# Kernel optimization log

Hardware: AMD Instinct MI355X
Metric: run time of the kernel (lower is better)

Reference implementation:

```python
import jax, jax.numpy as jnp
import numpy as np

D_MODEL = 128
EXPAND = 8
D_INNER = EXPAND * D_MODEL            # 1024
HEADDIM = D_MODEL                     # headdim = int(in_channels*8/8)
NHEADS = D_INNER // HEADDIM           # 8
D_STATE = 128
D_CONV = 4
CONV_DIM = D_INNER + 2 * D_STATE      # 1280
D_IN_PROJ = 2 * D_INNER + 2 * D_STATE + NHEADS  # 2312
EPS = 1e-5
B_SZ, SEQ = 2, 2048


def setup_inputs() -> dict:
    key = jax.random.key(0)
    ks = jax.random.split(key, 16)
    n = jax.random.normal
    dt_init = jax.random.uniform(ks[4], (NHEADS,), minval=0.001, maxval=0.1)
    return dict(
        hidden_states=n(ks[0], (B_SZ, SEQ, D_MODEL), jnp.float32),
        w_in=n(ks[1], (D_IN_PROJ, D_MODEL), jnp.float32) / np.float32(np.sqrt(D_MODEL)),
        conv_w=n(ks[2], (CONV_DIM, D_CONV), jnp.float32) / np.float32(np.sqrt(D_CONV)),
        conv_b=n(ks[3], (CONV_DIM,), jnp.float32) * 0.01,
        dt_bias=jnp.log(jnp.expm1(dt_init)),  # inverse-softplus init (official)
        A_log=jnp.log(jax.random.uniform(ks[5], (NHEADS,), minval=1.0, maxval=16.0)),
        D_skip=jnp.ones((NHEADS,), jnp.float32),
        gnorm_w=jnp.ones((D_INNER,), jnp.float32),
        w_out=n(ks[6], (D_MODEL, D_INNER), jnp.float32) / np.float32(np.sqrt(D_INNER)),
        ln1_w=jnp.ones((D_MODEL,), jnp.float32),
        ln1_b=jnp.zeros((D_MODEL,), jnp.float32),
        ln2_w=jnp.ones((D_MODEL,), jnp.float32),
        ln2_b=jnp.zeros((D_MODEL,), jnp.float32),
        mlp_w=n(ks[7], (D_MODEL, D_MODEL), jnp.float32) / np.float32(np.sqrt(D_MODEL)),
        mlp_b=jnp.zeros((D_MODEL,), jnp.float32),
    )


def _layer_norm(x, w, b):
    m = x.mean(-1, keepdims=True)
    xc = x - m
    v = (xc * xc).mean(-1, keepdims=True)
    return xc * jax.lax.rsqrt(v + EPS) * w + b


def _mixer(u, w_in, conv_w, conv_b, dt_bias, A_log, D_skip, gnorm_w, w_out):
    b, l, _ = u.shape
    zxbcdt = u @ w_in.T                                    # (b,l,2312)
    z = zxbcdt[..., :D_INNER]                              # gate
    xBC = zxbcdt[..., D_INNER:D_INNER + CONV_DIM]
    dt = jax.nn.softplus(zxbcdt[..., -NHEADS:] + dt_bias)  # (b,l,h)
    # depthwise causal conv1d + SiLU
    xc = jnp.pad(xBC.swapaxes(1, 2), ((0, 0), (0, 0), (D_CONV - 1, 0)))
    xc = jax.lax.conv_general_dilated(xc, conv_w[:, None, :], (1,), 'VALID',
                                      feature_group_count=CONV_DIM)
    xBC = jax.nn.silu((xc + conv_b[None, :, None]).swapaxes(1, 2))
    x = xBC[..., :D_INNER].reshape(b, l, NHEADS, HEADDIM)  # (b,l,h,p)
    Bm = xBC[..., D_INNER:D_INNER + D_STATE]               # (b,l,n), ngroups=1
    Cm = xBC[..., D_INNER + D_STATE:]                      # (b,l,n)
    A = -jnp.exp(A_log)                                    # (h,)
    dA = jnp.exp(dt * A)                                   # (b,l,h)

    def step(S, inp):
        dA_t, dt_t, B_t, C_t, x_t = inp
        S = S * dA_t[:, :, None, None] + jnp.einsum('bh,bhp,bn->bhpn', dt_t, x_t, B_t)
        return S, jnp.einsum('bhpn,bn->bhp', S, C_t)

    S0 = jnp.zeros((b, NHEADS, HEADDIM, D_STATE), u.dtype)
    _, ys = jax.lax.scan(step, S0, (dA.swapaxes(0, 1), dt.swapaxes(0, 1),
                                    Bm.swapaxes(0, 1), Cm.swapaxes(0, 1),
                                    x.swapaxes(0, 1)))
    y = ys.swapaxes(0, 1) + D_skip[None, None, :, None] * x  # skip connection
    y = y.reshape(b, l, D_INNER) * jax.nn.silu(z)            # gated RMSNorm
    y = y * jax.lax.rsqrt((y * y).mean(-1, keepdims=True) + EPS) * gnorm_w
    return y @ w_out.T


def reference(hidden_states, w_in, conv_w, conv_b, dt_bias, A_log, D_skip,
              gnorm_w, w_out, ln1_w, ln1_b, ln2_w, ln2_b, mlp_w, mlp_b):
    residual = hidden_states
    h = _layer_norm(residual, ln1_w, ln1_b)
    h = _mixer(h, w_in, conv_w, conv_b, dt_bias, A_log, D_skip, gnorm_w, w_out)
    residual = h + residual
    h = _layer_norm(residual, ln2_w, ln2_b)
    return h @ mlp_w.T + mlp_b
```

## Files before the change

kernel.cpp:

```cpp
#include <hip/hip_runtime.h>
#include <hip/hip_bf16.h>

#define B_SZ 2
#define SEQ 2048
#define DMODEL 128
#define DINNER 1024
#define NHEADS 8
#define HEADDIM 128
#define DSTATE 128
#define CONVDIM 1280
#define NPROJ 2304
#define NTOK (B_SZ*SEQ)
#define CHUNK 64
#define NCHUNK (SEQ/CHUNK)
#define LDT 72

using bf16_t = __hip_bfloat16;
using short8 = __attribute__((ext_vector_type(8))) short;
using short4v= __attribute__((ext_vector_type(4))) short;
using f32x4  = __attribute__((ext_vector_type(4))) float;

__device__ __forceinline__ float silu_f(float x) { return x / (1.f + expf(-x)); }
__device__ __forceinline__ float bf2f(short s) {
    unsigned u = ((unsigned)(unsigned short)s) << 16;
    return __uint_as_float(u);
}
__device__ __forceinline__ short f2bf_s(float f) {
    bf16_t h = __float2bfloat16(f);
    return *(short*)&h;
}

__global__ __launch_bounds__(256) void cast3(const float* __restrict__ a, int na,
                                             const float* __restrict__ b, int nb,
                                             const float* __restrict__ c, int nc,
                                             bf16_t* __restrict__ oa,
                                             bf16_t* __restrict__ ob,
                                             bf16_t* __restrict__ oc) {
    int i = blockIdx.x * 256 + threadIdx.x;
    if (i < na) oa[i] = __float2bfloat16(a[i]);
    else if (i < na + nb) ob[i - na] = __float2bfloat16(b[i - na]);
    else if (i < na + nb + nc) oc[i - na - nb] = __float2bfloat16(c[i - na - nb]);
}

__global__ __launch_bounds__(128) void ln_ker(const float* __restrict__ x,
                                              const float* __restrict__ w,
                                              const float* __restrict__ b,
                                              float* __restrict__ out_f,
                                              bf16_t* __restrict__ out_b) {
    int m = blockIdx.x, t = threadIdx.x;
    __shared__ float red[128];
    float v = x[(size_t)m*DMODEL + t];
    red[t] = v; __syncthreads();
    for (int s = 64; s > 0; s >>= 1) { if (t < s) red[t] += red[t+s]; __syncthreads(); }
    float mean = red[0] * (1.f/128.f);
    __syncthreads();
    float xc = v - mean;
    red[t] = xc * xc; __syncthreads();
    for (int s = 64; s > 0; s >>= 1) { if (t < s) red[t] += red[t+s]; __syncthreads(); }
    float var = red[0] * (1.f/128.f);
    float o = xc * rsqrtf(var + 1e-5f) * w[t] + b[t];
    out_f[(size_t)m*DMODEL + t] = o;
    out_b[(size_t)m*DMODEL + t] = __float2bfloat16(o);
}

__global__ __launch_bounds__(256) void gemm_bf(const bf16_t* __restrict__ A,
                                               const bf16_t* __restrict__ W,
                                               bf16_t* __restrict__ C,
                                               int M, int N, int K) {
    int tid = threadIdx.x;
    int wave = tid >> 6, lane = tid & 63;
    int m0 = blockIdx.x * 64 + wave * 16;
    int n0 = blockIdx.y * 64;
    int lr = lane & 15, quad = lane >> 4;
    f32x4 acc[4];
#pragma unroll
    for (int j = 0; j < 4; j++) acc[j] = (f32x4){0.f, 0.f, 0.f, 0.f};
    for (int k0 = 0; k0 < K; k0 += 32) {
        short8 a = *(const short8*)(A + (size_t)(m0 + lr)*K + k0 + quad*8);
#pragma unroll
        for (int j = 0; j < 4; j++) {
            short8 b = *(const short8*)(W + (size_t)(n0 + j*16 + lr)*K + k0 + quad*8);
            acc[j] = __builtin_amdgcn_mfma_f32_16x16x32_bf16(a, b, acc[j], 0, 0, 0);
        }
    }
#pragma unroll
    for (int j = 0; j < 4; j++)
#pragma unroll
        for (int r = 0; r < 4; r++) {
            int row = m0 + quad*4 + r;
            int col = n0 + j*16 + lr;
            C[(size_t)row*N + col] = __float2bfloat16(acc[j][r]);
        }
}

__global__ __launch_bounds__(256) void dt_ker(const float* __restrict__ h,
                                              const float* __restrict__ w_in,
                                              const float* __restrict__ dt_bias,
                                              const float* __restrict__ A_log,
                                              float* __restrict__ dt,
                                              float* __restrict__ ldA) {
    int idx = blockIdx.x * 256 + threadIdx.x;
    if (idx >= NTOK * NHEADS) return;
    int m = idx >> 3, hd = idx & 7;
    const float* hr = h + (size_t)m * DMODEL;
    const float* wr = w_in + (size_t)(NPROJ + hd) * DMODEL;
    float s = 0.f;
#pragma unroll 8
    for (int k = 0; k < DMODEL; k++) s += hr[k] * wr[k];
    s += dt_bias[hd];
    float dtv = (s > 20.f) ? s : log1pf(expf(s));
    float Av = -expf(A_log[hd]);
    dt[idx] = dtv;
    ldA[idx] = dtv * Av;
}

__global__ __launch_bounds__(256) void conv_silu(const bf16_t* __restrict__ zxb,
                                                 const float* __restrict__ conv_w,
                                                 const float* __restrict__ conv_b,
                                                 bf16_t* __restrict__ xBCb) {
    int idx = blockIdx.x * 256 + threadIdx.x;
    if (idx >= NTOK * CONVDIM / 4) return;
    int c4 = (idx % (CONVDIM/4)) * 4;
    int m  = idx / (CONVDIM/4);
    int b = m >> 11, l = m & (SEQ - 1);
    float acc[4];
    f32x4 wv[4];
#pragma unroll
    for (int j = 0; j < 4; j++) {
        acc[j] = conv_b[c4 + j];
        wv[j] = *(const f32x4*)(conv_w + (c4 + j)*4);
    }
#pragma unroll
    for (int k = 0; k < 4; k++) {
        int ll = l - 3 + k;
        if (ll >= 0) {
            short4v v = *(const short4v*)(zxb + (size_t)(b*SEQ + ll)*NPROJ + DINNER + c4);
#pragma unroll
            for (int j = 0; j < 4; j++) acc[j] += bf2f(v[j]) * wv[j][k];
        }
    }
    short4v res;
#pragma unroll
    for (int j = 0; j < 4; j++) res[j] = f2bf_s(silu_f(acc[j]));
    *(short4v*)(xBCb + (size_t)m*CONVDIM + c4) = res;
}

__global__ __launch_bounds__(256) void scanA_mfma(const bf16_t* __restrict__ xBCb,
                                                  const float* __restrict__ dt,
                                                  const float* __restrict__ ldA,
                                                  bf16_t* __restrict__ Sloc,
                                                  float* __restrict__ Pbuf) {
    int bid = blockIdx.x;
    int c = bid & 31, hd = (bid >> 5) & 7, b = bid >> 8;
    int t = threadIdx.x, wave = t >> 6, lane = t & 63;
    int lr = lane & 15, quad = lane >> 4;
    __shared__ bf16_t XT[128*LDT];
    __shared__ bf16_t BT[128*LDT];
    __shared__ float ws[CHUNK];
    int m0tok = b*SEQ + c*CHUNK;
    if (t < 64) {
        float L = ldA[(m0tok + t)*NHEADS + hd];
#pragma unroll
        for (int d = 1; d < 64; d <<= 1) {
            float u = __shfl_up(L, d, 64);
            if (lane >= d) L += u;
        }
        float Ltot = __shfl(L, 63, 64);
        ws[t] = expf(Ltot - L) * dt[(m0tok + t)*NHEADS + hd];
        if (t == 63) Pbuf[bid] = expf(Ltot);
    }
    __syncthreads();
#pragma unroll 4
    for (int i = 0; i < 32; i++) {
        int idx = i*256 + t;
        int tt = idx >> 7, p = idx & 127;
        const bf16_t* row = xBCb + (size_t)(m0tok + tt)*CONVDIM;
        float xv = bf2f(*(const short*)&row[hd*HEADDIM + p]);
        XT[p*LDT + tt] = __float2bfloat16(xv * ws[tt]);
        BT[p*LDT + tt] = row[DINNER + p];
    }
    __syncthreads();
    int m0w = wave * 32;
    f32x4 acc[2][8];
#pragma unroll
    for (int mi = 0; mi < 2; mi++)
#pragma unroll
        for (int ni = 0; ni < 8; ni++) acc[mi][ni] = (f32x4){0.f,0.f,0.f,0.f};
#pragma unroll
    for (int k0 = 0; k0 < 64; k0 += 32) {
        short8 a[2];
#pragma unroll
        for (int mi = 0; mi < 2; mi++)
            a[mi] = *(const short8*)&XT[(m0w + mi*16 + lr)*LDT + k0 + quad*8];
#pragma unroll
        for (int ni = 0; ni < 8; ni++) {
            short8 bb = *(const short8*)&BT[(ni*16 + lr)*LDT + k0 + quad*8];
#pragma unroll
            for (int mi = 0; mi < 2; mi++)
                acc[mi][ni] = __builtin_amdgcn_mfma_f32_16x16x32_bf16(a[mi], bb, acc[mi][ni], 0, 0, 0);
        }
    }
    bf16_t* outp = Sloc + (size_t)bid * 16384;
#pragma unroll
    for (int mi = 0; mi < 2; mi++)
#pragma unroll
        for (int ni = 0; ni < 8; ni++)
#pragma unroll
            for (int r = 0; r < 4; r++) {
                int p = m0w + mi*16 + quad*4 + r;
                int n = ni*16 + lr;
                outp[p*128 + n] = __float2bfloat16(acc[mi][ni][r]);
            }
}

__global__ __launch_bounds__(256) void scanB(const bf16_t* __restrict__ Sloc,
                                             bf16_t* __restrict__ Sini,
                                             const float* __restrict__ Pbuf) {
    int bid = blockIdx.x;
    int s = bid & 15, hd = (bid >> 4) & 7, b = bid >> 7;
    int t = threadIdx.x;
    int off = s*1024 + t*4;
    size_t base = (size_t)(b*NHEADS + hd) * NCHUNK * 16384;
    float run[4] = {0.f, 0.f, 0.f, 0.f};
    for (int c = 0; c < NCHUNK; c++) {
        short4v raw = *(const short4v*)(Sloc + base + (size_t)c*16384 + off);
        float P = Pbuf[(b*NHEADS + hd)*NCHUNK + c];
        short4v outv;
#pragma unroll
        for (int i = 0; i < 4; i++) {
            outv[i] = f2bf_s(run[i]);
            run[i] = run[i]*P + bf2f(raw[i]);
        }
        *(short4v*)(Sini + base + (size_t)c*16384 + off) = outv;
    }
}

__global__ __launch_bounds__(256) void scanC_mfma(const bf16_t* __restrict__ xBCb,
                                                  const float* __restrict__ dt,
                                                  const float* __restrict__ ldA,
                                                  const bf16_t* __restrict__ Sini,
                                                  const float* __restrict__ Dskip,
                                                  float* __restrict__ ybuf) {
    int bid = blockIdx.x;
    int c = bid & 31, hd = (bid >> 5) & 7, b = bid >> 8;
    int t = threadIdx.x, wave = t >> 6, lane = t & 63;
    int lr = lane & 15, quad = lane >> 4;
    __shared__ bf16_t XT[128*LDT];
    __shared__ bf16_t Mlds[64*LDT];
    __shared__ float Ls[CHUNK], dts[CHUNK];
    int m0tok = b*SEQ + c*CHUNK;
    if (t < 64) {
        float L = ldA[(m0tok + t)*NHEADS + hd];
#pragma unroll
        for (int d = 1; d < 64; d <<= 1) {
            float u = __shfl_up(L, d, 64);
            if (lane >= d) L += u;
        }
        Ls[t] = L;
        dts[t] = dt[(m0tok + t)*NHEADS + hd];
    }
#pragma unroll 4
    for (int i = 0; i < 32; i++) {
        int idx = i*256 + t;
        int tt = idx >> 7, p = idx & 127;
        XT[p*LDT + tt] = xBCb[(size_t)(m0tok + tt)*CONVDIM + hd*HEADDIM + p];
    }
    __syncthreads();
    const bf16_t* Crow = xBCb + (size_t)m0tok*CONVDIM + DINNER + DSTATE;
    const bf16_t* Brow = xBCb + (size_t)m0tok*CONVDIM + DINNER;
    f32x4 g[4];
#pragma unroll
    for (int si = 0; si < 4; si++) g[si] = (f32x4){0.f,0.f,0.f,0.f};
#pragma unroll
    for (int k0 = 0; k0 < 128; k0 += 32) {
        short8 a = *(const short8*)(Crow + (size_t)(wave*16 + lr)*CONVDIM + k0 + quad*8);
#pragma unroll
        for (int si = 0; si < 4; si++) {
            short8 bb = *(const short8*)(Brow + (size_t)(si*16 + lr)*CONVDIM + k0 + quad*8);
            g[si] = __builtin_amdgcn_mfma_f32_16x16x32_bf16(a, bb, g[si], 0, 0, 0);
        }
    }
#pragma unroll
    for (int si = 0; si < 4; si++)
#pragma unroll
        for (int r = 0; r < 4; r++) {
            int tt = wave*16 + quad*4 + r;
            int ss = si*16 + lr;
            float v = (ss <= tt) ? g[si][r] * expf(Ls[tt] - Ls[ss]) * dts[ss] : 0.f;
            Mlds[tt*LDT + ss] = __float2bfloat16(v);
        }
    __syncthreads();
    int p0 = wave * 32;
    f32x4 acc[4][2];
#pragma unroll
    for (int mi = 0; mi < 4; mi++)
#pragma unroll
        for (int ni = 0; ni < 2; ni++) acc[mi][ni] = (f32x4){0.f,0.f,0.f,0.f};
    const bf16_t* Sb = Sini + (size_t)bid * 16384;
#pragma unroll
    for (int k0 = 0; k0 < 128; k0 += 32) {
        short8 aC[4];
#pragma unroll
        for (int mi = 0; mi < 4; mi++)
            aC[mi] = *(const short8*)(Crow + (size_t)(mi*16 + lr)*CONVDIM + k0 + quad*8);
#pragma unroll
        for (int ni = 0; ni < 2; ni++) {
            short8 bb = *(const short8*)(Sb + (size_t)(p0 + ni*16 + lr)*128 + k0 + quad*8);
#pragma unroll
            for (int mi = 0; mi < 4; mi++)
                acc[mi][ni] = __builtin_amdgcn_mfma_f32_16x16x32_bf16(aC[mi], bb, acc[mi][ni], 0, 0, 0);
        }
    }
#pragma unroll
    for (int mi = 0; mi < 4; mi++) {
        float el[4];
#pragma unroll
        for (int r = 0; r < 4; r++) el[r] = expf(Ls[mi*16 + quad*4 + r]);
#pragma unroll
        for (int ni = 0; ni < 2; ni++)
#pragma unroll
            for (int r = 0; r < 4; r++) acc[mi][ni][r] *= el[r];
    }
#pragma unroll
    for (int k0 = 0; k0 < 64; k0 += 32) {
        short8 aM[4];
#pragma unroll
        for (int mi = 0; mi < 4; mi++)
            aM[mi] = *(const short8*)&Mlds[(mi*16 + lr)*LDT + k0 + quad*8];
#pragma unroll
        for (int ni = 0; ni < 2; ni++) {
            short8 bb = *(const short8*)&XT[(p0 + ni*16 + lr)*LDT + k0 + quad*8];
#pragma unroll
            for (int mi = 0; mi < 4; mi++)
                acc[mi][ni] = __builtin_amdgcn_mfma_f32_16x16x32_bf16(aM[mi], bb, acc[mi][ni], 0, 0, 0);
        }
    }
    float dsk = Dskip[hd];
#pragma unroll
    for (int mi = 0; mi < 4; mi++)
#pragma unroll
        for (int ni = 0; ni < 2; ni++)
#pragma unroll
            for (int r = 0; r < 4; r++) {
                int tt = mi*16 + quad*4 + r;
                int pp = p0 + ni*16 + lr;
                float xv = bf2f(*(const short*)&XT[pp*LDT + tt]);
                int m = m0tok + tt;
                ybuf[(size_t)m*DINNER + hd*HEADDIM + pp] = acc[mi][ni][r] + dsk*xv;
            }
}

__global__ __launch_bounds__(256) void gate_out(const float* __restrict__ ybuf,
                                                const bf16_t* __restrict__ zxb,
                                                const float* __restrict__ gw,
                                                const bf16_t* __restrict__ Wb,
                                                float* __restrict__ mix) {
    int blk = blockIdx.x, t = threadIdx.x;
    int tok0 = blk * 16;
    int tt = t >> 4, cg = t & 15;
    int ch0 = cg * 64;
    __shared__ bf16_t A[16*1032];
    float vals[64];
    const float*  yr = ybuf + (size_t)(tok0 + tt)*DINNER + ch0;
    const bf16_t* zr = zxb  + (size_t)(tok0 + tt)*NPROJ  + ch0;
    float ss = 0.f;
#pragma unroll
    for (int i = 0; i < 64; i += 4) {
        f32x4 y = *(const f32x4*)(yr + i);
        short4v z = *(const short4v*)(zr + i);
#pragma unroll
        for (int r = 0; r < 4; r++) {
            float v = y[r] * silu_f(bf2f(z[r]));
            vals[i + r] = v; ss += v*v;
        }
    }
#pragma unroll
    for (int d = 1; d < 16; d <<= 1) ss += __shfl_xor(ss, d, 64);
    float rstd = rsqrtf(ss*(1.f/1024.f) + 1e-5f);
#pragma unroll
    for (int i = 0; i < 64; i += 4) {
        short4v pk;
#pragma unroll
        for (int r = 0; r < 4; r++) pk[r] = f2bf_s(vals[i+r]*rstd*gw[ch0+i+r]);
        *(short4v*)&A[tt*1032 + ch0 + i] = pk;
    }
    __syncthreads();
    int wave = t >> 6, lane = t & 63, lr = lane & 15, quad = lane >> 4;
    f32x4 acc[2];
    acc[0] = (f32x4){0.f,0.f,0.f,0.f}; acc[1] = (f32x4){0.f,0.f,0.f,0.f};
    for (int k0 = 0; k0 < 1024; k0 += 32) {
        short8 a = *(const short8*)&A[lr*1032 + k0 + quad*8];
#pragma unroll
        for (int j = 0; j < 2; j++) {
            int col = wave*32 + j*16 + lr;
            short8 bb = *(const short8*)(Wb + (size_t)col*DINNER + k0 + quad*8);
            acc[j] = __builtin_amdgcn_mfma_f32_16x16x32_bf16(a, bb, acc[j], 0, 0, 0);
        }
    }
#pragma unroll
    for (int j = 0; j < 2; j++)
#pragma unroll
        for (int r = 0; r < 4; r++) {
            int row = tok0 + quad*4 + r;
            int col = wave*32 + j*16 + lr;
            mix[(size_t)row*DMODEL + col] = acc[j][r];
        }
}

__global__ __launch_bounds__(256) void ln_mlp(const float* __restrict__ mix,
                                              const float* __restrict__ resid,
                                              const float* __restrict__ w,
                                              const float* __restrict__ b,
                                              const bf16_t* __restrict__ Wm,
                                              const float* __restrict__ mb,
                                              float* __restrict__ out) {
    int blk = blockIdx.x, t = threadIdx.x;
    int tok0 = blk * 16;
    int tt = t >> 4, cg = t & 15;
    int ch0 = cg * 8;
    __shared__ bf16_t A[16*136];
    const float* xr = mix   + (size_t)(tok0 + tt)*DMODEL + ch0;
    const float* rr = resid + (size_t)(tok0 + tt)*DMODEL + ch0;
    float v[8];
    {
        f32x4 x0 = *(const f32x4*)xr, x1 = *(const f32x4*)(xr + 4);
        f32x4 r0 = *(const f32x4*)rr, r1 = *(const f32x4*)(rr + 4);
#pragma unroll
        for (int r = 0; r < 4; r++) { v[r] = x0[r] + r0[r]; v[4+r] = x1[r] + r1[r]; }
    }
    float s = 0.f, sq = 0.f;
#pragma unroll
    for (int i = 0; i < 8; i++) { s += v[i]; sq += v[i]*v[i]; }
#pragma unroll
    for (int d = 1; d < 16; d <<= 1) { s += __shfl_xor(s, d, 64); sq += __shfl_xor(sq, d, 64); }
    float mean = s * (1.f/128.f);
    float var  = sq * (1.f/128.f) - mean*mean;
    float rstd = rsqrtf(var + 1e-5f);
    {
        short4v p0, p1;
#pragma unroll
        for (int r = 0; r < 4; r++) {
            p0[r] = f2bf_s((v[r]   - mean)*rstd*w[ch0+r]   + b[ch0+r]);
            p1[r] = f2bf_s((v[4+r] - mean)*rstd*w[ch0+4+r] + b[ch0+4+r]);
        }
        *(short4v*)&A[tt*136 + ch0]     = p0;
        *(short4v*)&A[tt*136 + ch0 + 4] = p1;
    }
    __syncthreads();
    int wave = t >> 6, lane = t & 63, lr = lane & 15, quad = lane >> 4;
    f32x4 acc[2];
    acc[0] = (f32x4){0.f,0.f,0.f,0.f}; acc[1] = (f32x4){0.f,0.f,0.f,0.f};
#pragma unroll
    for (int k0 = 0; k0 < 128; k0 += 32) {
        short8 a = *(const short8*)&A[lr*136 + k0 + quad*8];
#pragma unroll
        for (int j = 0; j < 2; j++) {
            int col = wave*32 + j*16 + lr;
            short8 bb = *(const short8*)(Wm + (size_t)col*DMODEL + k0 + quad*8);
            acc[j] = __builtin_amdgcn_mfma_f32_16x16x32_bf16(a, bb, acc[j], 0, 0, 0);
        }
    }
#pragma unroll
    for (int j = 0; j < 2; j++)
#pragma unroll
        for (int r = 0; r < 4; r++) {
            int row = tok0 + quad*4 + r;
            int col = wave*32 + j*16 + lr;
            out[(size_t)row*DMODEL + col] = acc[j][r] + mb[col];
        }
}

extern "C" void kernel_launch(void* const* d_in, const int* in_sizes, int n_in,
                              void* d_out, int out_size, void* d_ws, size_t ws_size,
                              hipStream_t stream) {
    const float* hidden  = (const float*)d_in[0];
    const float* w_in    = (const float*)d_in[1];
    const float* conv_w  = (const float*)d_in[2];
    const float* conv_b  = (const float*)d_in[3];
    const float* dt_bias = (const float*)d_in[4];
    const float* A_log   = (const float*)d_in[5];
    const float* D_skip  = (const float*)d_in[6];
    const float* gnorm_w = (const float*)d_in[7];
    const float* w_out   = (const float*)d_in[8];
    const float* ln1_w   = (const float*)d_in[9];
    const float* ln1_b   = (const float*)d_in[10];
    const float* ln2_w   = (const float*)d_in[11];
    const float* ln2_b   = (const float*)d_in[12];
    const float* mlp_w   = (const float*)d_in[13];
    const float* mlp_b   = (const float*)d_in[14];
    float* out = (float*)d_out;

    char* ws = (char*)d_ws;
    size_t off = 0;
    auto alloc = [&](size_t bytes) -> void* {
        void* p = ws + off;
        off = (off + bytes + 255) & ~(size_t)255;
        return p;
    };
    float*  h      = (float*) alloc((size_t)NTOK*DMODEL*4);
    bf16_t* h_bf   = (bf16_t*)alloc((size_t)NTOK*DMODEL*2);
    bf16_t* w_in_bf= (bf16_t*)alloc((size_t)NPROJ*DMODEL*2);
    bf16_t* w_out_bf=(bf16_t*)alloc((size_t)DMODEL*DINNER*2);
    bf16_t* mlp_bf = (bf16_t*)alloc((size_t)DMODEL*DMODEL*2);
    bf16_t* zx_bf  = (bf16_t*)alloc((size_t)NTOK*NPROJ*2);
    bf16_t* xBCb   = (bf16_t*)alloc((size_t)NTOK*CONVDIM*2);
    float*  dtb    = (float*) alloc((size_t)NTOK*NHEADS*4);
    float*  ldAb   = (float*) alloc((size_t)NTOK*NHEADS*4);
    bf16_t* Sloc   = (bf16_t*)alloc((size_t)B_SZ*NHEADS*NCHUNK*16384*2);
    bf16_t* Sini   = (bf16_t*)alloc((size_t)B_SZ*NHEADS*NCHUNK*16384*2);
    float*  Pbuf   = (float*) alloc((size_t)B_SZ*NHEADS*NCHUNK*4);
    float*  ybuf   = (float*) alloc((size_t)NTOK*DINNER*4);
    float*  mix    = (float*) alloc((size_t)NTOK*DMODEL*4);
    (void)ws_size; (void)in_sizes; (void)n_in; (void)out_size;

    {
        int na = NPROJ*DMODEL, nb = DMODEL*DINNER, nc = DMODEL*DMODEL;
        cast3<<<(na+nb+nc + 255)/256, 256, 0, stream>>>(w_in, na, w_out, nb, mlp_w, nc,
                                                        w_in_bf, w_out_bf, mlp_bf);
    }
    ln_ker<<<NTOK, 128, 0, stream>>>(hidden, ln1_w, ln1_b, h, h_bf);
    gemm_bf<<<dim3(NTOK/64, NPROJ/64), 256, 0, stream>>>(h_bf, w_in_bf, zx_bf,
                                                         NTOK, NPROJ, DMODEL);
    dt_ker<<<(NTOK*NHEADS + 255)/256, 256, 0, stream>>>(h, w_in, dt_bias, A_log, dtb, ldAb);
    conv_silu<<<((size_t)NTOK*CONVDIM/4 + 255)/256, 256, 0, stream>>>(zx_bf, conv_w, conv_b, xBCb);
    scanA_mfma<<<B_SZ*NHEADS*NCHUNK, 256, 0, stream>>>(xBCb, dtb, ldAb, Sloc, Pbuf);
    scanB<<<B_SZ*NHEADS*16, 256, 0, stream>>>(Sloc, Sini, Pbuf);
    scanC_mfma<<<B_SZ*NHEADS*NCHUNK, 256, 0, stream>>>(xBCb, dtb, ldAb, Sini, D_skip, ybuf);
    gate_out<<<NTOK/16, 256, 0, stream>>>(ybuf, zx_bf, gnorm_w, w_out_bf, mix);
    ln_mlp<<<NTOK/16, 256, 0, stream>>>(mix, hidden, ln2_w, ln2_b, mlp_bf, mlp_b, out);
}
```

Measured before the change: 189.0 us.

## Fuse causal conv+SiLU into scan kernels and widen scanB parallelism

Removes the standalone conv_silu kernel and its xBC intermediate buffer. scanA and scanC now each recompute the depthwise causal conv and SiLU for their chunk directly from the projection output, and scanC stages B and C in LDS instead of reading them from global memory. scanB is split into twice as many blocks, each handling two elements per thread, to raise parallelism. The trade-off is redundant conv work: B and C are recomputed by every head and by both scan kernels. LDS use in scanC also grows, and it is given a launch bound of two blocks per SM.

```diff
diff --git a/kernel.cpp b/kernel.cpp
--- a/kernel.cpp
+++ b/kernel.cpp
@@ -14,6 +14,7 @@
 #define CHUNK 64
 #define NCHUNK (SEQ/CHUNK)
 #define LDT 72
+#define LDN 136
 
 using bf16_t = __hip_bfloat16;
 using short8 = __attribute__((ext_vector_type(8))) short;
@@ -114,38 +115,31 @@
     ldA[idx] = dtv * Av;
 }
 
-__global__ __launch_bounds__(256) void conv_silu(const bf16_t* __restrict__ zxb,
-                                                 const float* __restrict__ conv_w,
-                                                 const float* __restrict__ conv_b,
-                                                 bf16_t* __restrict__ xBCb) {
-    int idx = blockIdx.x * 256 + threadIdx.x;
-    if (idx >= NTOK * CONVDIM / 4) return;
-    int c4 = (idx % (CONVDIM/4)) * 4;
-    int m  = idx / (CONVDIM/4);
-    int b = m >> 11, l = m & (SEQ - 1);
-    float acc[4];
+__device__ __forceinline__ void conv4(const bf16_t* __restrict__ zxb,
+                                      const float* __restrict__ conv_w,
+                                      const float* __restrict__ conv_b,
+                                      int b, int l, int ch, float acc[4]) {
     f32x4 wv[4];
 #pragma unroll
     for (int j = 0; j < 4; j++) {
-        acc[j] = conv_b[c4 + j];
-        wv[j] = *(const f32x4*)(conv_w + (c4 + j)*4);
-    }
+        acc[j] = conv_b[ch + j];
+        wv[j] = *(const f32x4*)(conv_w + (ch + j)*4);
+    }
+    int zcol = DINNER + ch;
 #pragma unroll
     for (int k = 0; k < 4; k++) {
         int ll = l - 3 + k;
         if (ll >= 0) {
-            short4v v = *(const short4v*)(zxb + (size_t)(b*SEQ + ll)*NPROJ + DINNER + c4);
+            short4v v = *(const short4v*)(zxb + (size_t)(b*SEQ + ll)*NPROJ + zcol);
 #pragma unroll
             for (int j = 0; j < 4; j++) acc[j] += bf2f(v[j]) * wv[j][k];
         }
     }
-    short4v res;
-#pragma unroll
-    for (int j = 0; j < 4; j++) res[j] = f2bf_s(silu_f(acc[j]));
-    *(short4v*)(xBCb + (size_t)m*CONVDIM + c4) = res;
-}
-
-__global__ __launch_bounds__(256) void scanA_mfma(const bf16_t* __restrict__ xBCb,
+}
+
+__global__ __launch_bounds__(256) void scanA_conv(const bf16_t* __restrict__ zxb,
+                                                  const float* __restrict__ conv_w,
+                                                  const float* __restrict__ conv_b,
                                                   const float* __restrict__ dt,
                                                   const float* __restrict__ ldA,
                                                   bf16_t* __restrict__ Sloc,
@@ -158,6 +152,7 @@
     __shared__ bf16_t BT[128*LDT];
     __shared__ float ws[CHUNK];
     int m0tok = b*SEQ + c*CHUNK;
+    int l0 = c*CHUNK;
     if (t < 64) {
         float L = ldA[(m0tok + t)*NHEADS + hd];
 #pragma unroll
@@ -170,14 +165,25 @@
         if (t == 63) Pbuf[bid] = expf(Ltot);
     }
     __syncthreads();
-#pragma unroll 4
-    for (int i = 0; i < 32; i++) {
-        int idx = i*256 + t;
-        int tt = idx >> 7, p = idx & 127;
-        const bf16_t* row = xBCb + (size_t)(m0tok + tt)*CONVDIM;
-        float xv = bf2f(*(const short*)&row[hd*HEADDIM + p]);
-        XT[p*LDT + tt] = __float2bfloat16(xv * ws[tt]);
-        BT[p*LDT + tt] = row[DINNER + p];
+#pragma unroll 2
+    for (int i = 0; i < 16; i++) {
+        int u = i*256 + t;
+        int tt = u & 63;
+        int cg2 = u >> 6;
+        bool isX = cg2 < 32;
+        int ch = isX ? hd*HEADDIM + cg2*4 : DINNER + (cg2 - 32)*4;
+        float acc[4];
+        conv4(zxb, conv_w, conv_b, b, l0 + tt, ch, acc);
+        if (isX) {
+            float w_t = ws[tt];
+#pragma unroll
+            for (int j = 0; j < 4; j++)
+                XT[(cg2*4 + j)*LDT + tt] = __float2bfloat16(silu_f(acc[j]) * w_t);
+        } else {
+#pragma unroll
+            for (int j = 0; j < 4; j++)
+                BT[((cg2-32)*4 + j)*LDT + tt] = __float2bfloat16(silu_f(acc[j]));
+        }
     }
     __syncthreads();
     int m0w = wave * 32;
@@ -217,38 +223,41 @@
                                              bf16_t* __restrict__ Sini,
                                              const float* __restrict__ Pbuf) {
     int bid = blockIdx.x;
-    int s = bid & 15, hd = (bid >> 4) & 7, b = bid >> 7;
+    int bh = bid >> 5, slice = bid & 31;
     int t = threadIdx.x;
-    int off = s*1024 + t*4;
-    size_t base = (size_t)(b*NHEADS + hd) * NCHUNK * 16384;
-    float run[4] = {0.f, 0.f, 0.f, 0.f};
-    for (int c = 0; c < NCHUNK; c++) {
-        short4v raw = *(const short4v*)(Sloc + base + (size_t)c*16384 + off);
-        float P = Pbuf[(b*NHEADS + hd)*NCHUNK + c];
-        short4v outv;
-#pragma unroll
-        for (int i = 0; i < 4; i++) {
-            outv[i] = f2bf_s(run[i]);
-            run[i] = run[i]*P + bf2f(raw[i]);
-        }
-        *(short4v*)(Sini + base + (size_t)c*16384 + off) = outv;
-    }
-}
-
-__global__ __launch_bounds__(256) void scanC_mfma(const bf16_t* __restrict__ xBCb,
-                                                  const float* __restrict__ dt,
-                                                  const float* __restrict__ ldA,
-                                                  const bf16_t* __restrict__ Sini,
-                                                  const float* __restrict__ Dskip,
-                                                  float* __restrict__ ybuf) {
+    int off = slice*512 + t*2;
+    size_t base = (size_t)bh * NCHUNK * 16384;
+    float run0 = 0.f, run1 = 0.f;
+    for (int cc = 0; cc < NCHUNK; cc++) {
+        unsigned raw = *(const unsigned*)(Sloc + base + (size_t)cc*16384 + off);
+        float P = Pbuf[bh*NCHUNK + cc];
+        unsigned o0 = (unsigned)(unsigned short)f2bf_s(run0);
+        unsigned o1 = (unsigned)(unsigned short)f2bf_s(run1);
+        *(unsigned*)(Sini + base + (size_t)cc*16384 + off) = o0 | (o1 << 16);
+        run0 = run0*P + bf2f((short)(raw & 0xffff));
+        run1 = run1*P + bf2f((short)(raw >> 16));
+    }
+}
+
+__global__ __launch_bounds__(256, 2) void scanC_conv(const bf16_t* __restrict__ zxb,
+                                                     const float* __restrict__ conv_w,
+                                                     const float* __restrict__ conv_b,
+                                                     const float* __restrict__ dt,
+                                                     const float* __restrict__ ldA,
+                                                     const bf16_t* __restrict__ Sini,
+                                                     const float* __restrict__ Dskip,
+                                                     float* __restrict__ ybuf) {
     int bid = blockIdx.x;
     int c = bid & 31, hd = (bid >> 5) & 7, b = bid >> 8;
     int t = threadIdx.x, wave = t >> 6, lane = t & 63;
     int lr = lane & 15, quad = lane >> 4;
     __shared__ bf16_t XT[128*LDT];
     __shared__ bf16_t Mlds[64*LDT];
+    __shared__ bf16_t Ct[64*LDN];
+    __shared__ bf16_t Bt[64*LDN];
     __shared__ float Ls[CHUNK], dts[CHUNK];
     int m0tok = b*SEQ + c*CHUNK;
+    int l0 = c*CHUNK;
     if (t < 64) {
         float L = ldA[(m0tok + t)*NHEADS + hd];
 #pragma unroll
@@ -259,24 +268,39 @@
         Ls[t] = L;
         dts[t] = dt[(m0tok + t)*NHEADS + hd];
     }
-#pragma unroll 4
-    for (int i = 0; i < 32; i++) {
-        int idx = i*256 + t;
-        int tt = idx >> 7, p = idx & 127;
-        XT[p*LDT + tt] = xBCb[(size_t)(m0tok + tt)*CONVDIM + hd*HEADDIM + p];
-    }
-    __syncthreads();
-    const bf16_t* Crow = xBCb + (size_t)m0tok*CONVDIM + DINNER + DSTATE;
-    const bf16_t* Brow = xBCb + (size_t)m0tok*CONVDIM + DINNER;
+#pragma unroll 2
+    for (int i = 0; i < 24; i++) {
+        int u = i*256 + t;
+        int tt = u & 63;
+        int cg2 = u >> 6;
+        int ch;
+        if (cg2 < 32)      ch = hd*HEADDIM + cg2*4;
+        else if (cg2 < 64) ch = DINNER + (cg2 - 32)*4;
+        else               ch = DINNER + DSTATE + (cg2 - 64)*4;
+        float acc[4];
+        conv4(zxb, conv_w, conv_b, b, l0 + tt, ch, acc);
+        if (cg2 < 32) {
+#pragma unroll
+            for (int j = 0; j < 4; j++)
+                XT[(cg2*4 + j)*LDT + tt] = __float2bfloat16(silu_f(acc[j]));
+        } else {
+            short4v pk;
+#pragma unroll
+            for (int j = 0; j < 4; j++) pk[j] = f2bf_s(silu_f(acc[j]));
+            if (cg2 < 64) *(short4v*)&Bt[tt*LDN + (cg2-32)*4] = pk;
+            else          *(short4v*)&Ct[tt*LDN + (cg2-64)*4] = pk;
+        }
+    }
+    __syncthreads();
     f32x4 g[4];
 #pragma unroll
     for (int si = 0; si < 4; si++) g[si] = (f32x4){0.f,0.f,0.f,0.f};
 #pragma unroll
     for (int k0 = 0; k0 < 128; k0 += 32) {
-        short8 a = *(const short8*)(Crow + (size_t)(wave*16 + lr)*CONVDIM + k0 + quad*8);
+        short8 a = *(const short8*)&Ct[(wave*16 + lr)*LDN + k0 + quad*8];
 #pragma unroll
         for (int si = 0; si < 4; si++) {
-            short8 bb = *(const short8*)(Brow + (size_t)(si*16 + lr)*CONVDIM + k0 + quad*8);
+            short8 bb = *(const short8*)&Bt[(si*16 + lr)*LDN + k0 + quad*8];
             g[si] = __builtin_amdgcn_mfma_f32_16x16x32_bf16(a, bb, g[si], 0, 0, 0);
         }
     }
@@ -302,7 +326,7 @@
         short8 aC[4];
 #pragma unroll
         for (int mi = 0; mi < 4; mi++)
-            aC[mi] = *(const short8*)(Crow + (size_t)(mi*16 + lr)*CONVDIM + k0 + quad*8);
+            aC[mi] = *(const short8*)&Ct[(mi*16 + lr)*LDN + k0 + quad*8];
 #pragma unroll
         for (int ni = 0; ni < 2; ni++) {
             short8 bb = *(const short8*)(Sb + (size_t)(p0 + ni*16 + lr)*128 + k0 + quad*8);
@@ -503,7 +527,6 @@
     bf16_t* w_out_bf=(bf16_t*)alloc((size_t)DMODEL*DINNER*2);
     bf16_t* mlp_bf = (bf16_t*)alloc((size_t)DMODEL*DMODEL*2);
     bf16_t* zx_bf  = (bf16_t*)alloc((size_t)NTOK*NPROJ*2);
-    bf16_t* xBCb   = (bf16_t*)alloc((size_t)NTOK*CONVDIM*2);
     float*  dtb    = (float*) alloc((size_t)NTOK*NHEADS*4);
     float*  ldAb   = (float*) alloc((size_t)NTOK*NHEADS*4);
     bf16_t* Sloc   = (bf16_t*)alloc((size_t)B_SZ*NHEADS*NCHUNK*16384*2);
@@ -522,10 +545,11 @@
     gemm_bf<<<dim3(NTOK/64, NPROJ/64), 256, 0, stream>>>(h_bf, w_in_bf, zx_bf,
                                                          NTOK, NPROJ, DMODEL);
     dt_ker<<<(NTOK*NHEADS + 255)/256, 256, 0, stream>>>(h, w_in, dt_bias, A_log, dtb, ldAb);
-    conv_silu<<<((size_t)NTOK*CONVDIM/4 + 255)/256, 256, 0, stream>>>(zx_bf, conv_w, conv_b, xBCb);
-    scanA_mfma<<<B_SZ*NHEADS*NCHUNK, 256, 0, stream>>>(xBCb, dtb, ldAb, Sloc, Pbuf);
-    scanB<<<B_SZ*NHEADS*16, 256, 0, stream>>>(Sloc, Sini, Pbuf);
-    scanC_mfma<<<B_SZ*NHEADS*NCHUNK, 256, 0, stream>>>(xBCb, dtb, ldAb, Sini, D_skip, ybuf);
+    scanA_conv<<<B_SZ*NHEADS*NCHUNK, 256, 0, stream>>>(zx_bf, conv_w, conv_b, dtb, ldAb,
+                                                       Sloc, Pbuf);
+    scanB<<<B_SZ*NHEADS*NCHUNK, 256, 0, stream>>>(Sloc, Sini, Pbuf);
+    scanC_conv<<<B_SZ*NHEADS*NCHUNK, 256, 0, stream>>>(zx_bf, conv_w, conv_b, dtb, ldAb,
+                                                       Sini, D_skip, ybuf);
     gate_out<<<NTOK/16, 256, 0, stream>>>(ybuf, zx_bf, gnorm_w, w_out_bf, mix);
     ln_mlp<<<NTOK/16, 256, 0, stream>>>(mix, hidden, ln2_w, ln2_b, mlp_bf, mlp_b, out);
 }
```

Result: slower. 218.3 us (+15.5%).

## Fuse weight cast, LayerNorm and dt projection into one kernel; widen scanB grid

Applied to the files above, without the earlier changes.

Merges the weight bf16 cast, the first LayerNorm and the dt projection/softplus into a single launch, with extra blocks handling the cast. The dt dot product now uses wave shuffles on the normalized row, so the fp32 h buffer is no longer written or re-read. scanB gets twice as many blocks, each handling two elements per thread, to expose more parallelism in the inter-chunk scan. This removes two launches and some traffic, at the cost of a heterogeneous kernel with divergent block roles.

```diff
diff --git a/kernel.cpp b/kernel.cpp
--- a/kernel.cpp
+++ b/kernel.cpp
@@ -30,26 +30,27 @@
     return *(short*)&h;
 }
 
-__global__ __launch_bounds__(256) void cast3(const float* __restrict__ a, int na,
-                                             const float* __restrict__ b, int nb,
-                                             const float* __restrict__ c, int nc,
-                                             bf16_t* __restrict__ oa,
-                                             bf16_t* __restrict__ ob,
-                                             bf16_t* __restrict__ oc) {
-    int i = blockIdx.x * 256 + threadIdx.x;
-    if (i < na) oa[i] = __float2bfloat16(a[i]);
-    else if (i < na + nb) ob[i - na] = __float2bfloat16(b[i - na]);
-    else if (i < na + nb + nc) oc[i - na - nb] = __float2bfloat16(c[i - na - nb]);
-}
-
-__global__ __launch_bounds__(128) void ln_ker(const float* __restrict__ x,
-                                              const float* __restrict__ w,
-                                              const float* __restrict__ b,
-                                              float* __restrict__ out_f,
-                                              bf16_t* __restrict__ out_b) {
-    int m = blockIdx.x, t = threadIdx.x;
+__global__ __launch_bounds__(128) void head_fused(
+        const float* __restrict__ hidden,
+        const float* __restrict__ ln1_w, const float* __restrict__ ln1_b,
+        const float* __restrict__ w_in,
+        const float* __restrict__ dt_bias, const float* __restrict__ A_log,
+        bf16_t* __restrict__ h_bf, float* __restrict__ dtb, float* __restrict__ ldAb,
+        const float* __restrict__ wa, int na, const float* __restrict__ wb, int nb,
+        const float* __restrict__ wc, int nc,
+        bf16_t* __restrict__ oa, bf16_t* __restrict__ ob, bf16_t* __restrict__ oc) {
+    int blk = blockIdx.x;
+    if (blk >= NTOK) {
+        int i = (blk - NTOK) * 128 + threadIdx.x;
+        if (i < na) oa[i] = __float2bfloat16(wa[i]);
+        else if (i < na + nb) ob[i - na] = __float2bfloat16(wb[i - na]);
+        else if (i < na + nb + nc) oc[i - na - nb] = __float2bfloat16(wc[i - na - nb]);
+        return;
+    }
+    int m = blk, t = threadIdx.x;
     __shared__ float red[128];
-    float v = x[(size_t)m*DMODEL + t];
+    __shared__ float sred[2][8];
+    float v = hidden[(size_t)m*DMODEL + t];
     red[t] = v; __syncthreads();
     for (int s = 64; s > 0; s >>= 1) { if (t < s) red[t] += red[t+s]; __syncthreads(); }
     float mean = red[0] * (1.f/128.f);
@@ -58,9 +59,24 @@
     red[t] = xc * xc; __syncthreads();
     for (int s = 64; s > 0; s >>= 1) { if (t < s) red[t] += red[t+s]; __syncthreads(); }
     float var = red[0] * (1.f/128.f);
-    float o = xc * rsqrtf(var + 1e-5f) * w[t] + b[t];
-    out_f[(size_t)m*DMODEL + t] = o;
-    out_b[(size_t)m*DMODEL + t] = __float2bfloat16(o);
+    float o = xc * rsqrtf(var + 1e-5f) * ln1_w[t] + ln1_b[t];
+    h_bf[(size_t)m*DMODEL + t] = __float2bfloat16(o);
+    int wave = t >> 6, lane = t & 63;
+#pragma unroll
+    for (int hd = 0; hd < NHEADS; hd++) {
+        float p = o * w_in[(size_t)(NPROJ + hd)*DMODEL + t];
+#pragma unroll
+        for (int d = 1; d < 64; d <<= 1) p += __shfl_xor(p, d, 64);
+        if (lane == 0) sred[wave][hd] = p;
+    }
+    __syncthreads();
+    if (t < NHEADS) {
+        float s = sred[0][t] + sred[1][t] + dt_bias[t];
+        float dtv = (s > 20.f) ? s : log1pf(expf(s));
+        float Av = -expf(A_log[t]);
+        dtb[m*NHEADS + t] = dtv;
+        ldAb[m*NHEADS + t] = dtv * Av;
+    }
 }
 
 __global__ __launch_bounds__(256) void gemm_bf(const bf16_t* __restrict__ A,
@@ -91,27 +107,6 @@
             int col = n0 + j*16 + lr;
             C[(size_t)row*N + col] = __float2bfloat16(acc[j][r]);
         }
-}
-
-__global__ __launch_bounds__(256) void dt_ker(const float* __restrict__ h,
-                                              const float* __restrict__ w_in,
-                                              const float* __restrict__ dt_bias,
-                                              const float* __restrict__ A_log,
-                                              float* __restrict__ dt,
-                                              float* __restrict__ ldA) {
-    int idx = blockIdx.x * 256 + threadIdx.x;
-    if (idx >= NTOK * NHEADS) return;
-    int m = idx >> 3, hd = idx & 7;
-    const float* hr = h + (size_t)m * DMODEL;
-    const float* wr = w_in + (size_t)(NPROJ + hd) * DMODEL;
-    float s = 0.f;
-#pragma unroll 8
-    for (int k = 0; k < DMODEL; k++) s += hr[k] * wr[k];
-    s += dt_bias[hd];
-    float dtv = (s > 20.f) ? s : log1pf(expf(s));
-    float Av = -expf(A_log[hd]);
-    dt[idx] = dtv;
-    ldA[idx] = dtv * Av;
 }
 
 __global__ __launch_bounds__(256) void conv_silu(const bf16_t* __restrict__ zxb,
@@ -217,21 +212,19 @@
                                              bf16_t* __restrict__ Sini,
                                              const float* __restrict__ Pbuf) {
     int bid = blockIdx.x;
-    int s = bid & 15, hd = (bid >> 4) & 7, b = bid >> 7;
+    int bh = bid >> 5, slice = bid & 31;
     int t = threadIdx.x;
-    int off = s*1024 + t*4;
-    size_t base = (size_t)(b*NHEADS + hd) * NCHUNK * 16384;
-    float run[4] = {0.f, 0.f, 0.f, 0.f};
-    for (int c = 0; c < NCHUNK; c++) {
-        short4v raw = *(const short4v*)(Sloc + base + (size_t)c*16384 + off);
-        float P = Pbuf[(b*NHEADS + hd)*NCHUNK + c];
-        short4v outv;
-#pragma unroll
-        for (int i = 0; i < 4; i++) {
-            outv[i] = f2bf_s(run[i]);
-            run[i] = run[i]*P + bf2f(raw[i]);
-        }
-        *(short4v*)(Sini + base + (size_t)c*16384 + off) = outv;
+    int off = slice*512 + t*2;
+    size_t base = (size_t)bh * NCHUNK * 16384;
+    float run0 = 0.f, run1 = 0.f;
+    for (int cc = 0; cc < NCHUNK; cc++) {
+        unsigned raw = *(const unsigned*)(Sloc + base + (size_t)cc*16384 + off);
+        float P = Pbuf[bh*NCHUNK + cc];
+        unsigned o0 = (unsigned)(unsigned short)f2bf_s(run0);
+        unsigned o1 = (unsigned)(unsigned short)f2bf_s(run1);
+        *(unsigned*)(Sini + base + (size_t)cc*16384 + off) = o0 | (o1 << 16);
+        run0 = run0*P + bf2f((short)(raw & 0xffff));
+        run1 = run1*P + bf2f((short)(raw >> 16));
     }
 }
 
@@ -497,7 +490,6 @@
         off = (off + bytes + 255) & ~(size_t)255;
         return p;
     };
-    float*  h      = (float*) alloc((size_t)NTOK*DMODEL*4);
     bf16_t* h_bf   = (bf16_t*)alloc((size_t)NTOK*DMODEL*2);
     bf16_t* w_in_bf= (bf16_t*)alloc((size_t)NPROJ*DMODEL*2);
     bf16_t* w_out_bf=(bf16_t*)alloc((size_t)DMODEL*DINNER*2);
@@ -515,16 +507,16 @@
 
     {
         int na = NPROJ*DMODEL, nb = DMODEL*DINNER, nc = DMODEL*DMODEL;
-        cast3<<<(na+nb+nc + 255)/256, 256, 0, stream>>>(w_in, na, w_out, nb, mlp_w, nc,
-                                                        w_in_bf, w_out_bf, mlp_bf);
-    }
-    ln_ker<<<NTOK, 128, 0, stream>>>(hidden, ln1_w, ln1_b, h, h_bf);
+        int castBlocks = (na + nb + nc + 127) / 128;
+        head_fused<<<NTOK + castBlocks, 128, 0, stream>>>(
+            hidden, ln1_w, ln1_b, w_in, dt_bias, A_log, h_bf, dtb, ldAb,
+            w_in, na, w_out, nb, mlp_w, nc, w_in_bf, w_out_bf, mlp_bf);
+    }
     gemm_bf<<<dim3(NTOK/64, NPROJ/64), 256, 0, stream>>>(h_bf, w_in_bf, zx_bf,
                                                          NTOK, NPROJ, DMODEL);
-    dt_ker<<<(NTOK*NHEADS + 255)/256, 256, 0, stream>>>(h, w_in, dt_bias, A_log, dtb, ldAb);
     conv_silu<<<((size_t)NTOK*CONVDIM/4 + 255)/256, 256, 0, stream>>>(zx_bf, conv_w, conv_b, xBCb);
     scanA_mfma<<<B_SZ*NHEADS*NCHUNK, 256, 0, stream>>>(xBCb, dtb, ldAb, Sloc, Pbuf);
-    scanB<<<B_SZ*NHEADS*16, 256, 0, stream>>>(Sloc, Sini, Pbuf);
+    scanB<<<B_SZ*NHEADS*NCHUNK, 256, 0, stream>>>(Sloc, Sini, Pbuf);
     scanC_mfma<<<B_SZ*NHEADS*NCHUNK, 256, 0, stream>>>(xBCb, dtb, ldAb, Sini, D_skip, ybuf);
     gate_out<<<NTOK/16, 256, 0, stream>>>(ybuf, zx_bf, gnorm_w, w_out_bf, mix);
     ln_mlp<<<NTOK/16, 256, 0, stream>>>(mix, hidden, ln2_w, ln2_b, mlp_bf, mlp_b, out);
```

After: 185.3 us, median of 2. -2.0%, faster.
